# Performance work log

Measured on AMD Instinct MI355X. Metric: run time of the kernel, lower is better.

The kernel has to match this reference:

```python
import jax, jax.numpy as jnp
import numpy as np

N = 100000
E = 3200000
IN_F = 256
ATT_D = 128  # attention_dim, heads=1 so d_k = 128
SLOPE = 0.2  # leaky_relu_slope


def setup_inputs() -> dict:
    key = jax.random.key(0)
    k1, k2, k3, k4 = jax.random.split(key, 4)
    x = jax.random.normal(k1, (N, IN_F), dtype=jnp.float32)
    edge = jax.random.randint(k2, (2, E), 0, N, dtype=jnp.int64)
    # xavier_normal_ with gain=1.414 for W [in_features, attention_dim]
    std_W = 1.414 * np.sqrt(2.0 / (IN_F + ATT_D))
    W = jax.random.normal(k3, (IN_F, ATT_D), dtype=jnp.float32) * std_W
    # a has shape [2*d_k, 1, 1]; store flattened [2*d_k]
    std_a = 1.414 * np.sqrt(2.0 / (2 * ATT_D + 1))
    a = jax.random.normal(k4, (2 * ATT_D,), dtype=jnp.float32) * std_a
    return {"x": x, "edge": edge, "W": W, "a": a}


def reference(x, edge, W, a):
    d_k = W.shape[1]
    h = x @ W  # [N, d_k]  (heads=1, so h.view(-1,1,d_k).transpose is just [N, d_k, 1])
    # score_e = sum(a * cat(h[src], h[dst])) = (h @ a_src)[src] + (h @ a_dst)[dst]
    s_src = h @ a[:d_k]   # [N]
    s_dst = h @ a[d_k:]   # [N]
    src, dst = edge[0], edge[1]
    score = s_src[src] + s_dst[dst]                     # [E]
    score = jnp.where(score >= 0, score, SLOPE * score)  # LeakyReLU
    # segment softmax grouped by edge[attention_norm_idx] = edge[0]
    seg = src
    n = x.shape[0]
    m = jax.ops.segment_max(score, seg, num_segments=n)  # [N]
    ex = jnp.exp(score - m[seg])                          # [E]
    denom = jax.ops.segment_sum(ex, seg, num_segments=n)  # [N]
    att = ex / (denom[seg] + 1e-16)
    return att[:, None]  # [E, 1] matching edge_e shape
```

## Files before the change

### kernel.cpp

```cpp
#include <hip/hip_runtime.h>

constexpr int N    = 100000;
constexpr int E    = 3200000;
constexpr int IN_F = 256;
constexpr int D    = 128;
constexpr float SLOPE = 0.2f;

constexpr int R     = 8;
constexpr int RANGE = 12512;
constexpr int T     = 1024;

__global__ void k_wvec(const float* __restrict__ W, const float* __restrict__ a,
                       float* __restrict__ wsrc, float* __restrict__ wdst) {
    int i = threadIdx.x;
    const float* row = W + i * D;
    float s1 = 0.f, s2 = 0.f;
    #pragma unroll 8
    for (int j = 0; j < D; ++j) {
        float w = row[j];
        s1 += w * a[j];
        s2 += w * a[D + j];
    }
    wsrc[i] = s1;
    wdst[i] = s2;
}

__global__ void k_node(const float* __restrict__ x,
                       const float* __restrict__ wsrc,
                       const float* __restrict__ wdst,
                       float* __restrict__ ssrc, float* __restrict__ sdst) {
    int wave = blockIdx.x * (blockDim.x >> 6) + (threadIdx.x >> 6);
    int lane = threadIdx.x & 63;
    if (wave >= N) return;
    float4 xv = reinterpret_cast<const float4*>(x + (size_t)wave * IN_F)[lane];
    float4 w1 = reinterpret_cast<const float4*>(wsrc)[lane];
    float4 w2 = reinterpret_cast<const float4*>(wdst)[lane];
    float s1 = xv.x * w1.x + xv.y * w1.y + xv.z * w1.z + xv.w * w1.w;
    float s2 = xv.x * w2.x + xv.y * w2.y + xv.z * w2.z + xv.w * w2.w;
    #pragma unroll
    for (int off = 32; off; off >>= 1) {
        s1 += __shfl_xor(s1, off, 64);
        s2 += __shfl_xor(s2, off, 64);
    }
    if (lane == 0) {
        ssrc[wave] = s1;
        sdst[wave] = s2;
    }
}

__device__ __forceinline__ float edge_ex(float ss, float sd) {
    float sc = ss + sd;
    sc = (sc >= 0.f) ? sc : SLOPE * sc;
    return __expf(sc);
}

__global__ void __launch_bounds__(T) k_sum(
        const int* __restrict__ src, const int* __restrict__ dst,
        const float* __restrict__ ssrc, const float* __restrict__ sdst,
        float* __restrict__ part, float* __restrict__ exv, int B, int slice) {
    __shared__ float bins[RANGE];
    const int r    = blockIdx.x / B;
    const int b    = blockIdx.x % B;
    const int base = r * RANGE;
    const int hi   = min(base + RANGE, N);

    for (int i = threadIdx.x; i < RANGE; i += T) bins[i] = 0.f;
    __syncthreads();

    const int e0 = b * slice;
    const int e1 = min(e0 + slice, E);
    const int nvec = (e1 - e0) >> 2;
    const int4* s4p = reinterpret_cast<const int4*>(src + e0);
    const int4* d4p = reinterpret_cast<const int4*>(dst + e0);
    for (int v = threadIdx.x; v < nvec; v += T) {
        int4 s4 = s4p[v];
        int4 d4 = d4p[v];
        int  e  = e0 + 4 * v;
        if (s4.x >= base && s4.x < hi) {
            float ex = edge_ex(ssrc[s4.x], sdst[d4.x]);
            exv[e] = ex;
            atomicAdd(&bins[s4.x - base], ex);
        }
        if (s4.y >= base && s4.y < hi) {
            float ex = edge_ex(ssrc[s4.y], sdst[d4.y]);
            exv[e + 1] = ex;
            atomicAdd(&bins[s4.y - base], ex);
        }
        if (s4.z >= base && s4.z < hi) {
            float ex = edge_ex(ssrc[s4.z], sdst[d4.z]);
            exv[e + 2] = ex;
            atomicAdd(&bins[s4.z - base], ex);
        }
        if (s4.w >= base && s4.w < hi) {
            float ex = edge_ex(ssrc[s4.w], sdst[d4.w]);
            exv[e + 3] = ex;
            atomicAdd(&bins[s4.w - base], ex);
        }
    }
    __syncthreads();

    float* out = part + (size_t)b * N + base;
    for (int i = threadIdx.x; i < hi - base; i += T) out[i] = bins[i];
}

__global__ void k_comb(const float* __restrict__ part,
                       float* __restrict__ denom, int B) {
    int n4 = blockIdx.x * blockDim.x + threadIdx.x;
    if (n4 >= N / 4) return;
    float4 acc = {0.f, 0.f, 0.f, 0.f};
    for (int b = 0; b < B; ++b) {
        float4 p = reinterpret_cast<const float4*>(part + (size_t)b * N)[n4];
        acc.x += p.x; acc.y += p.y; acc.z += p.z; acc.w += p.w;
    }
    reinterpret_cast<float4*>(denom)[n4] = acc;
}

__global__ void k_out(const int* __restrict__ src,
                      const float* __restrict__ exv,
                      const float* __restrict__ denom, float* __restrict__ out) {
    int v = blockIdx.x * blockDim.x + threadIdx.x;
    if (v >= E / 4) return;
    int4   s4 = reinterpret_cast<const int4*>(src)[v];
    float4 e4 = reinterpret_cast<const float4*>(exv)[v];
    float4 o;
    o.x = e4.x / (denom[s4.x] + 1e-16f);
    o.y = e4.y / (denom[s4.y] + 1e-16f);
    o.z = e4.z / (denom[s4.z] + 1e-16f);
    o.w = e4.w / (denom[s4.w] + 1e-16f);
    reinterpret_cast<float4*>(out)[v] = o;
}

extern "C" void kernel_launch(void* const* d_in, const int* in_sizes, int n_in,
                              void* d_out, int out_size, void* d_ws, size_t ws_size,
                              hipStream_t stream) {
    const float* x    = (const float*)d_in[0];
    const int*   edge = (const int*)d_in[1];
    const float* W    = (const float*)d_in[2];
    const float* a    = (const float*)d_in[3];

    const int* src = edge;
    const int* dst = edge + E;

    size_t avail = ws_size / 4;
    size_t fixed = 512 + 3 * (size_t)N + (size_t)E;
    int B = 64;
    if (avail < fixed + (size_t)B * N) {
        long fit = (long)((avail - fixed) / N);
        B = (int)(fit & ~7L);
        if (B < 8) B = 8;
    }
    int slice = (((E + B - 1) / B) + 3) & ~3;

    float* ws    = (float*)d_ws;
    float* wsrc  = ws;
    float* wdst  = ws + 256;
    float* ssrc  = ws + 512;
    float* sdst  = ssrc + N;
    float* denom = sdst + N;
    float* exv   = denom + N;
    float* part  = exv + E;

    k_wvec<<<1, 256, 0, stream>>>(W, a, wsrc, wdst);
    k_node<<<(N + 3) / 4, 256, 0, stream>>>(x, wsrc, wdst, ssrc, sdst);

    k_sum <<<R * B, T, 0, stream>>>(src, dst, ssrc, sdst, part, exv, B, slice);
    k_comb<<<(N / 4 + 255) / 256, 256, 0, stream>>>(part, denom, B);

    k_out<<<(E / 4 + 255) / 256, 256, 0, stream>>>(src, exv, denom,
                                                   (float*)d_out);
}
```

Before: 109.0 us.

## Split edge exp computation out of the range-binned histogram kernel

The fused kernel that computed each edge's exp score and accumulated it into per-range shared-memory bins is split in two. A new k_ex kernel reads src and dst once, gathers the node scores and writes exv with coalesced float4 stores. k_bin then only reads src and exv per range and does the shared-memory atomics. The range check is also reduced to a single unsigned compare. This removes divergent gathers and scattered exv writes inside the range loop. The cost is an extra kernel launch plus an extra full write and re-read of the exv array.

```diff
diff --git a/kernel.cpp b/kernel.cpp
--- a/kernel.cpp
+++ b/kernel.cpp
@@ -54,15 +54,31 @@
     return __expf(sc);
 }
 
-__global__ void __launch_bounds__(T) k_sum(
-        const int* __restrict__ src, const int* __restrict__ dst,
-        const float* __restrict__ ssrc, const float* __restrict__ sdst,
-        float* __restrict__ part, float* __restrict__ exv, int B, int slice) {
+__global__ void k_ex(const int* __restrict__ src, const int* __restrict__ dst,
+                     const float* __restrict__ ssrc,
+                     const float* __restrict__ sdst,
+                     float* __restrict__ exv) {
+    int v = blockIdx.x * blockDim.x + threadIdx.x;
+    if (v >= E / 4) return;
+    int4 s4 = reinterpret_cast<const int4*>(src)[v];
+    int4 d4 = reinterpret_cast<const int4*>(dst)[v];
+    float4 o;
+    o.x = edge_ex(ssrc[s4.x], sdst[d4.x]);
+    o.y = edge_ex(ssrc[s4.y], sdst[d4.y]);
+    o.z = edge_ex(ssrc[s4.z], sdst[d4.z]);
+    o.w = edge_ex(ssrc[s4.w], sdst[d4.w]);
+    reinterpret_cast<float4*>(exv)[v] = o;
+}
+
+__global__ void __launch_bounds__(T) k_bin(
+        const int* __restrict__ src, const float* __restrict__ exv,
+        float* __restrict__ part, int B, int slice) {
     __shared__ float bins[RANGE];
     const int r    = blockIdx.x / B;
     const int b    = blockIdx.x % B;
     const int base = r * RANGE;
     const int hi   = min(base + RANGE, N);
+    const unsigned span = (unsigned)(hi - base);
 
     for (int i = threadIdx.x; i < RANGE; i += T) bins[i] = 0.f;
     __syncthreads();
@@ -70,32 +86,19 @@
     const int e0 = b * slice;
     const int e1 = min(e0 + slice, E);
     const int nvec = (e1 - e0) >> 2;
-    const int4* s4p = reinterpret_cast<const int4*>(src + e0);
-    const int4* d4p = reinterpret_cast<const int4*>(dst + e0);
+    const int4*   s4p = reinterpret_cast<const int4*>(src + e0);
+    const float4* e4p = reinterpret_cast<const float4*>(exv + e0);
     for (int v = threadIdx.x; v < nvec; v += T) {
-        int4 s4 = s4p[v];
-        int4 d4 = d4p[v];
-        int  e  = e0 + 4 * v;
-        if (s4.x >= base && s4.x < hi) {
-            float ex = edge_ex(ssrc[s4.x], sdst[d4.x]);
-            exv[e] = ex;
-            atomicAdd(&bins[s4.x - base], ex);
-        }
-        if (s4.y >= base && s4.y < hi) {
-            float ex = edge_ex(ssrc[s4.y], sdst[d4.y]);
-            exv[e + 1] = ex;
-            atomicAdd(&bins[s4.y - base], ex);
-        }
-        if (s4.z >= base && s4.z < hi) {
-            float ex = edge_ex(ssrc[s4.z], sdst[d4.z]);
-            exv[e + 2] = ex;
-            atomicAdd(&bins[s4.z - base], ex);
-        }
-        if (s4.w >= base && s4.w < hi) {
-            float ex = edge_ex(ssrc[s4.w], sdst[d4.w]);
-            exv[e + 3] = ex;
-            atomicAdd(&bins[s4.w - base], ex);
-        }
+        int4   s4 = s4p[v];
+        float4 e4 = e4p[v];
+        unsigned ix = (unsigned)(s4.x - base);
+        unsigned iy = (unsigned)(s4.y - base);
+        unsigned iz = (unsigned)(s4.z - base);
+        unsigned iw = (unsigned)(s4.w - base);
+        if (ix < span) atomicAdd(&bins[ix], e4.x);
+        if (iy < span) atomicAdd(&bins[iy], e4.y);
+        if (iz < span) atomicAdd(&bins[iz], e4.z);
+        if (iw < span) atomicAdd(&bins[iw], e4.w);
     }
     __syncthreads();
 
@@ -163,7 +166,8 @@
     k_wvec<<<1, 256, 0, stream>>>(W, a, wsrc, wdst);
     k_node<<<(N + 3) / 4, 256, 0, stream>>>(x, wsrc, wdst, ssrc, sdst);
 
-    k_sum <<<R * B, T, 0, stream>>>(src, dst, ssrc, sdst, part, exv, B, slice);
+    k_ex  <<<(E / 4 + 255) / 256, 256, 0, stream>>>(src, dst, ssrc, sdst, exv);
+    k_bin <<<R * B, T, 0, stream>>>(src, exv, part, B, slice);
     k_comb<<<(N / 4 + 255) / 256, 256, 0, stream>>>(part, denom, B);
 
     k_out<<<(E / 4 + 255) / 256, 256, 0, stream>>>(src, exv, denom,
```

Result: slower. 116.6 us (+7.0%).
